# Performance work log

Hardware: AMD Instinct MI355X
Metric: run time of the kernel (lower is better)

Reference implementation:

```python
import jax, jax.numpy as jnp
import numpy as np

N_NODES = 100000
N_EDGES = 1600000
F_IN = 256
EMB = 16  # conv1 out = 2*EMB = 32, conv2 out = EMB


def setup_inputs() -> dict:
    key = jax.random.key(0)
    k1, k2, k3, k4, k5, k6, k7 = jax.random.split(key, 7)
    x = jax.random.normal(k1, (N_NODES, F_IN), dtype=jnp.float32)
    edge_index = jax.random.randint(k2, (2, N_EDGES), 0, N_NODES, dtype=jnp.int64)
    edge_weight = jax.random.uniform(k3, (N_EDGES,), dtype=jnp.float32)
    # GCNConv params: glorot-ish weights, zero bias (materialized as params)
    s1 = 1.0 / np.sqrt(F_IN)
    s2 = 1.0 / np.sqrt(2 * EMB)
    W1 = jax.random.uniform(k4, (F_IN, 2 * EMB), minval=-s1, maxval=s1, dtype=jnp.float32)
    b1 = jnp.zeros((2 * EMB,), dtype=jnp.float32)
    W2 = jax.random.uniform(k5, (2 * EMB, EMB), minval=-s2, maxval=s2, dtype=jnp.float32)
    b2 = jnp.zeros((EMB,), dtype=jnp.float32)
    return {"x": x, "edge_index": edge_index, "edge_weight": edge_weight,
            "W1": W1, "b1": b1, "W2": W2, "b2": b2}


def _gcn_norm(edge_index, edge_weight, num_nodes, dtype):
    # PyG gcn_norm with add_self_loops=True, fill_value=1.0
    row, col = edge_index[0], edge_index[1]
    loop = jnp.arange(num_nodes)
    row_a = jnp.concatenate([row, loop])
    col_a = jnp.concatenate([col, loop])
    w_a = jnp.concatenate([edge_weight, jnp.ones((num_nodes,), dtype=dtype)])
    deg = jax.ops.segment_sum(w_a, col_a, num_segments=num_nodes)
    dinv = jnp.where(deg > 0, jax.lax.rsqrt(deg), jnp.zeros_like(deg))
    norm = dinv[row_a] * w_a * dinv[col_a]
    return row_a, col_a, norm


def _gcn_conv(x, W, b, row, col, norm, num_nodes):
    h = x @ W                                  # [N, d_out] dense projection
    msg = norm[:, None] * h[row]               # gather + edge scale, [E+N, d_out]
    out = jax.ops.segment_sum(msg, col, num_segments=num_nodes)  # scatter-add
    return out + b


def reference(x, edge_index, edge_weight, W1, b1, W2, b2):
    n = x.shape[0]
    row, col, norm = _gcn_norm(edge_index, edge_weight, n, x.dtype)
    h = jax.nn.relu(_gcn_conv(x, W1, b1, row, col, norm, n))
    return _gcn_conv(h, W2, b2, row, col, norm, n)
```

## Files before the change

### kernel.cpp

```cpp
#include <hip/hip_runtime.h>
#include <hip/hip_bf16.h>

#define NN   100000
#define NE   1600000
#define FIN  256
#define HID  32
#define OUTD 16
#define NBLK ((NN + 255) / 256)

#define BM          256
#define GEMM_BLOCKS ((NN + BM - 1) / BM)
#define CNT_EDGES   2048
#define CNT_BLOCKS  ((NE + CNT_EDGES - 1) / CNT_EDGES)
#define FUSE_BLOCKS (GEMM_BLOCKS + CNT_BLOCKS)
#define FILL_BLOCKS ((NE + 1023) / 1024)

#define OFF_FLAG    0
#define OFF_DEG     64
#define OFF_DINV    (OFF_DEG + NN)
#define OFF_RANK    (OFF_DINV + NN)
#define OFF_BSUM    (OFF_RANK + NE)
#define OFF_ROWPTR  (OFF_BSUM + 1024)
#define OFF_CSR     (OFF_ROWPTR + NN + 32)
#define OFF_H1      (OFF_CSR + 2*NE)
#define OFF_P2      (OFF_H1 + NN*HID)

#define CSHIFT 26
#define CMASK  ((1u << CSHIFT) - 1u)
#define WSCALE 1048576.0f
#define WINV   (1.0f / 1048576.0f)

__device__ __forceinline__ float bf2f(unsigned short u) {
  union { unsigned int i; float f; } v; v.i = ((unsigned int)u) << 16; return v.f;
}
__device__ __forceinline__ unsigned short f2bf(float f) {
  union { float f; unsigned int i; } v; v.f = f;
  unsigned int x = v.i;
  return (unsigned short)((x + 0x7fffu + ((x >> 16) & 1u)) >> 16);
}
__device__ __forceinline__ int eidx(const int* __restrict__ ei, long long pos, int is64) {
  return is64 ? ei[2 * pos] : ei[pos];
}
__device__ __forceinline__ float ldf(const void* p, long long i, int isf32) {
  return isf32 ? ((const float*)p)[i] : bf2f(((const unsigned short*)p)[i]);
}

__global__ __launch_bounds__(256) void detect_zero_kernel(const int* __restrict__ ei,
    const unsigned short* __restrict__ xu, int* __restrict__ flags,
    unsigned int* __restrict__ zp, int zn) {
  int b = blockIdx.x;
  if (b == 0) {
    __shared__ int any, cnt;
    if (threadIdx.x == 0) { any = 0; cnt = 0; }
    __syncthreads();
    int local = 0, c = 0;
    for (int i = threadIdx.x; i < 2048; i += 256) local |= ei[2 * i + 1];
    for (int i = threadIdx.x; i < 1024; i += 256) {
      unsigned int e = (xu[2 * i] >> 7) & 0xFF;
      c += (e < 100 || e > 140) ? 1 : 0;
    }
    if (local) atomicOr(&any, 1);
    atomicAdd(&cnt, c);
    __syncthreads();
    if (threadIdx.x == 0) {
      flags[0] = (any == 0) ? 1 : 0;
      flags[1] = (cnt > 100) ? 1 : 0;
    }
  } else {
    int stride = (gridDim.x - 1) * 256;
    for (int i = (b - 1) * 256 + threadIdx.x; i < zn; i += stride) zp[i] = 0u;
  }
}

__global__ __launch_bounds__(256, 4) void count_gemm_kernel(const int* __restrict__ ei,
    const void* __restrict__ ew, unsigned int* __restrict__ deg,
    int* __restrict__ rank, const void* __restrict__ x,
    const void* __restrict__ W1, float* __restrict__ h1,
    const int* __restrict__ flags) {
  __shared__ float xs[32][BM];
  __shared__ float wl[32][36];
  int b = blockIdx.x;
  int t = threadIdx.x;

  if ((b % 3) < 2) {
    int cid = (b / 3) * 2 + (b % 3);
    int is64 = flags[0], isf32 = flags[1];
    int e0 = cid * CNT_EDGES + t;
    int c[8]; float w[8];
    #pragma unroll
    for (int q = 0; q < 8; q++) {
      int e = e0 + q * 256;
      if (e < NE) {
        c[q] = eidx(ei, (long long)NE + e, is64);
        w[q] = ldf(ew, e, isf32);
      } else c[q] = -1;
    }
    unsigned int old[8];
    #pragma unroll
    for (int q = 0; q < 8; q++) {
      if (c[q] >= 0) {
        unsigned int inc = (1u << CSHIFT) | (unsigned int)(w[q] * WSCALE + 0.5f);
        old[q] = atomicAdd(deg + c[q], inc);
      }
    }
    #pragma unroll
    for (int q = 0; q < 8; q++)
      if (c[q] >= 0) rank[e0 + q * 256] = (int)(old[q] >> CSHIFT);
    return;
  }

  int gid = b / 3;
  int rb = gid * BM;
  int isf32 = flags[1];

  int rowg = t >> 3, colg = t & 7;
  int r0 = rowg * 8, m0 = colg * 4;
  int srow = t >> 1;
  int kk0s = (t & 1) * 16;
  int kkw = t >> 3, mw = (t & 7) * 4;

  float acc[8][4];
  #pragma unroll
  for (int i = 0; i < 8; i++)
    #pragma unroll
    for (int j = 0; j < 4; j++) acc[i][j] = 0.f;

  union Pf { uint4 u[4]; float f[16]; unsigned short s[32]; };
  Pf pfx[2];
  uint4 pw;

#define LOADX(rblk, kc_) do {                                                  \
    int row_ = srow + (rblk) * 128;                                            \
    long long g_ = (long long)rb + row_;                                       \
    if (g_ < NN) {                                                             \
      if (isf32) {                                                             \
        const float* xp_ = (const float*)x + g_ * FIN + (kc_) + kk0s;          \
        pfx[rblk].u[0] = ((const uint4*)xp_)[0];                               \
        pfx[rblk].u[1] = ((const uint4*)xp_)[1];                               \
        pfx[rblk].u[2] = ((const uint4*)xp_)[2];                               \
        pfx[rblk].u[3] = ((const uint4*)xp_)[3];                               \
      } else {                                                                 \
        const unsigned short* xp_ = (const unsigned short*)x + g_ * FIN + (kc_) + kk0s; \
        pfx[rblk].u[0] = ((const uint4*)xp_)[0];                               \
        pfx[rblk].u[1] = ((const uint4*)xp_)[1];                               \
      }                                                                        \
    }                                                                          \
  } while (0)

#define STOREX(rblk) do {                                                      \
    int row_ = srow + (rblk) * 128;                                            \
    bool ok_ = ((long long)rb + row_) < NN;                                    \
    if (isf32) {                                                               \
      _Pragma("unroll")                                                        \
      for (int q = 0; q < 16; q++) xs[kk0s + q][row_] = ok_ ? pfx[rblk].f[q] : 0.f; \
    } else {                                                                   \
      _Pragma("unroll")                                                        \
      for (int q = 0; q < 16; q++) xs[kk0s + q][row_] = ok_ ? bf2f(pfx[rblk].s[q]) : 0.f; \
    }                                                                          \
  } while (0)

#define LOADW(kc_) do {                                                        \
    if (isf32) {                                                               \
      pw = *(const uint4*)((const float*)W1 + ((kc_) + kkw) * HID + mw);       \
    } else {                                                                   \
      const unsigned short* wp_ = (const unsigned short*)W1 + ((kc_) + kkw) * HID + mw; \
      pw.x = ((const unsigned int*)wp_)[0];                                    \
      pw.y = ((const unsigned int*)wp_)[1];                                    \
    }                                                                          \
  } while (0)

#define STOREW() do {                                                          \
    if (isf32) {                                                               \
      *(float4*)&wl[kkw][mw] = *(float4*)&pw;                                  \
    } else {                                                                   \
      const unsigned short* ps_ = (const unsigned short*)&pw;                  \
      wl[kkw][mw + 0] = bf2f(ps_[0]); wl[kkw][mw + 1] = bf2f(ps_[1]);          \
      wl[kkw][mw + 2] = bf2f(ps_[2]); wl[kkw][mw + 3] = bf2f(ps_[3]);          \
    }                                                                          \
  } while (0)

  LOADX(0, 0); LOADX(1, 0); LOADW(0);

  for (int kc = 0; kc < FIN; kc += 32) {
    __syncthreads();
    STOREX(0); STOREX(1); STOREW();
    __syncthreads();
    if (kc + 32 < FIN) { LOADX(0, kc + 32); LOADX(1, kc + 32); LOADW(kc + 32); }
    #pragma unroll 8
    for (int kk = 0; kk < 32; kk++) {
      float4 xa = *(const float4*)&xs[kk][r0];
      float4 xb = *(const float4*)&xs[kk][r0 + 4];
      float4 wv = *(const float4*)&wl[kk][m0];
      float xr[8] = {xa.x, xa.y, xa.z, xa.w, xb.x, xb.y, xb.z, xb.w};
      float wr[4] = {wv.x, wv.y, wv.z, wv.w};
      #pragma unroll
      for (int i = 0; i < 8; i++)
        #pragma unroll
        for (int j = 0; j < 4; j++)
          acc[i][j] = fmaf(xr[i], wr[j], acc[i][j]);
    }
  }

  #pragma unroll
  for (int i = 0; i < 8; i++) {
    int g = rb + r0 + i;
    if (g < NN) {
      float4 v; v.x = acc[i][0]; v.y = acc[i][1]; v.z = acc[i][2]; v.w = acc[i][3];
      *(float4*)(h1 + (long long)g * HID + m0) = v;
    }
  }
#undef LOADX
#undef STOREX
#undef LOADW
#undef STOREW
}

__global__ __launch_bounds__(256) void dinv_scansum_kernel(
    const unsigned int* __restrict__ deg, float* __restrict__ dinv,
    int* __restrict__ bsum) {
  int b = blockIdx.x;
  if (b < NBLK) {
    __shared__ int s[256];
    int i = b * 256 + threadIdx.x;
    s[threadIdx.x] = (i < NN) ? (int)(deg[i] >> CSHIFT) : 0;
    __syncthreads();
    for (int off = 128; off > 0; off >>= 1) {
      if (threadIdx.x < off) s[threadIdx.x] += s[threadIdx.x + off];
      __syncthreads();
    }
    if (threadIdx.x == 0) bsum[b] = s[0];
  } else {
    int i = (b - NBLK) * 256 + threadIdx.x;
    if (i >= NN) return;
    float d = (float)(deg[i] & CMASK) * WINV + 1.0f;
    dinv[i] = rsqrtf(d);
  }
}

__global__ __launch_bounds__(256) void scan_write_kernel(const unsigned int* __restrict__ deg,
    const int* __restrict__ bsum, int* __restrict__ rowptr) {
  __shared__ int a[256];
  __shared__ int base_s;
  int t = threadIdx.x;
  int b = blockIdx.x;
  int v = 0;
  for (int i = t; i < NBLK; i += 256) v += (i < b) ? bsum[i] : 0;
  a[t] = v;
  __syncthreads();
  for (int off = 128; off > 0; off >>= 1) {
    if (t < off) a[t] += a[t + off];
    __syncthreads();
  }
  if (t == 0) base_s = a[0];
  __syncthreads();
  int base = base_s;
  int i = b * 256 + t;
  int orig = (i < NN) ? (int)(deg[i] >> CSHIFT) : 0;
  a[t] = orig;
  __syncthreads();
  for (int off = 1; off < 256; off <<= 1) {
    int x2 = a[t] + ((t >= off) ? a[t - off] : 0);
    __syncthreads();
    a[t] = x2;
    __syncthreads();
  }
  if (i < NN) rowptr[i] = base + a[t] - orig;
  if (b == 0 && t == 0) rowptr[NN] = NE;
}

__global__ __launch_bounds__(256) void fill_csr_kernel(const int* __restrict__ ei,
    const void* __restrict__ ew, const float* __restrict__ dinv,
    const int* __restrict__ rowptr, const int* __restrict__ rank,
    int2* __restrict__ csr, const int* __restrict__ flags) {
  int is64 = flags[0], isf32 = flags[1];
  int e0 = blockIdx.x * 1024 + threadIdx.x;
  int r[4], c[4], rk[4]; float w[4];
  #pragma unroll
  for (int q = 0; q < 4; q++) {
    int e = e0 + q * 256;
    if (e < NE) {
      r[q]  = eidx(ei, e, is64);
      c[q]  = eidx(ei, (long long)NE + e, is64);
      w[q]  = ldf(ew, e, isf32);
      rk[q] = rank[e];
    } else c[q] = -1;
  }
  float dr[4], dc[4]; int rp[4];
  #pragma unroll
  for (int q = 0; q < 4; q++) {
    if (c[q] >= 0) {
      dr[q] = dinv[r[q]];
      dc[q] = dinv[c[q]];
      rp[q] = rowptr[c[q]];
    }
  }
  #pragma unroll
  for (int q = 0; q < 4; q++) {
    if (c[q] >= 0) {
      int2 pr; pr.x = r[q]; pr.y = __float_as_int(dr[q] * w[q] * dc[q]);
      csr[rp[q] + rk[q]] = pr;
    }
  }
}

__global__ __launch_bounds__(256) void gather1_kernel(const float* __restrict__ h1,
    const float* __restrict__ dinv, const int* __restrict__ rowptr,
    const int2* __restrict__ csr, const void* __restrict__ b1,
    const void* __restrict__ W2, float* __restrict__ p2,
    const int* __restrict__ flags) {
  __shared__ float w2lds[HID * OUTD];
  __shared__ float b1l[HID];
  __shared__ float tl[8][HID + 1];
  int t = threadIdx.x;
  int isf32 = flags[1];
  w2lds[2 * t]     = ldf(W2, 2 * t, isf32);
  w2lds[2 * t + 1] = ldf(W2, 2 * t + 1, isf32);
  if (t < HID) b1l[t] = ldf(b1, t, isf32);
  __syncthreads();

  int nl = t >> 5;
  int j  = t & 31;
  int node = blockIdx.x * 8 + nl;
  if (node < NN) {
    int k0 = rowptr[node], k1 = rowptr[node + 1];
    float acc = 0.f;
    int k = k0;
    for (; k + 8 <= k1; k += 8) {
      int2 q0 = csr[k];     int2 q1 = csr[k + 1];
      int2 q2 = csr[k + 2]; int2 q3 = csr[k + 3];
      int2 q4 = csr[k + 4]; int2 q5 = csr[k + 5];
      int2 q6 = csr[k + 6]; int2 q7 = csr[k + 7];
      float v0 = h1[q0.x * HID + j]; float v1 = h1[q1.x * HID + j];
      float v2 = h1[q2.x * HID + j]; float v3 = h1[q3.x * HID + j];
      float v4 = h1[q4.x * HID + j]; float v5 = h1[q5.x * HID + j];
      float v6 = h1[q6.x * HID + j]; float v7 = h1[q7.x * HID + j];
      acc = fmaf(__int_as_float(q0.y), v0, acc);
      acc = fmaf(__int_as_float(q1.y), v1, acc);
      acc = fmaf(__int_as_float(q2.y), v2, acc);
      acc = fmaf(__int_as_float(q3.y), v3, acc);
      acc = fmaf(__int_as_float(q4.y), v4, acc);
      acc = fmaf(__int_as_float(q5.y), v5, acc);
      acc = fmaf(__int_as_float(q6.y), v6, acc);
      acc = fmaf(__int_as_float(q7.y), v7, acc);
    }
    for (; k + 4 <= k1; k += 4) {
      int2 q0 = csr[k];     int2 q1 = csr[k + 1];
      int2 q2 = csr[k + 2]; int2 q3 = csr[k + 3];
      float v0 = h1[q0.x * HID + j]; float v1 = h1[q1.x * HID + j];
      float v2 = h1[q2.x * HID + j]; float v3 = h1[q3.x * HID + j];
      acc = fmaf(__int_as_float(q0.y), v0, acc);
      acc = fmaf(__int_as_float(q1.y), v1, acc);
      acc = fmaf(__int_as_float(q2.y), v2, acc);
      acc = fmaf(__int_as_float(q3.y), v3, acc);
    }
    for (; k < k1; k++) {
      int2 pr = csr[k];
      acc = fmaf(__int_as_float(pr.y), h1[pr.x * HID + j], acc);
    }
    float di = dinv[node];
    acc = fmaf(di * di, h1[node * HID + j], acc);
    acc += b1l[j];
    tl[nl][j] = fmaxf(acc, 0.f);
  }
  __syncthreads();
  int m = t & 31;
  if (node < NN && m < OUTD) {
    float s = 0.f;
    #pragma unroll
    for (int k = 0; k < HID; k++) s = fmaf(tl[nl][k], w2lds[k * OUTD + m], s);
    p2[node * OUTD + m] = s;
  }
}

__global__ __launch_bounds__(256) void gather2_kernel(const float* __restrict__ p2,
    const float* __restrict__ dinv, const int* __restrict__ rowptr,
    const int2* __restrict__ csr, const void* __restrict__ b2,
    void* __restrict__ out, const int* __restrict__ flags) {
  __shared__ float b2l[OUTD];
  int t = threadIdx.x;
  int isf32 = flags[1];
  if (t < OUTD) b2l[t] = ldf(b2, t, isf32);
  __syncthreads();

  int nl = t >> 4;
  int m  = t & 15;
  int node = blockIdx.x * 16 + nl;
  if (node >= NN) return;
  int k0 = rowptr[node], k1 = rowptr[node + 1];
  float acc = 0.f;
  int k = k0;
  for (; k + 8 <= k1; k += 8) {
    int2 q0 = csr[k];     int2 q1 = csr[k + 1];
    int2 q2 = csr[k + 2]; int2 q3 = csr[k + 3];
    int2 q4 = csr[k + 4]; int2 q5 = csr[k + 5];
    int2 q6 = csr[k + 6]; int2 q7 = csr[k + 7];
    float v0 = p2[q0.x * OUTD + m]; float v1 = p2[q1.x * OUTD + m];
    float v2 = p2[q2.x * OUTD + m]; float v3 = p2[q3.x * OUTD + m];
    float v4 = p2[q4.x * OUTD + m]; float v5 = p2[q5.x * OUTD + m];
    float v6 = p2[q6.x * OUTD + m]; float v7 = p2[q7.x * OUTD + m];
    acc = fmaf(__int_as_float(q0.y), v0, acc);
    acc = fmaf(__int_as_float(q1.y), v1, acc);
    acc = fmaf(__int_as_float(q2.y), v2, acc);
    acc = fmaf(__int_as_float(q3.y), v3, acc);
    acc = fmaf(__int_as_float(q4.y), v4, acc);
    acc = fmaf(__int_as_float(q5.y), v5, acc);
    acc = fmaf(__int_as_float(q6.y), v6, acc);
    acc = fmaf(__int_as_float(q7.y), v7, acc);
  }
  for (; k + 4 <= k1; k += 4) {
    int2 q0 = csr[k];     int2 q1 = csr[k + 1];
    int2 q2 = csr[k + 2]; int2 q3 = csr[k + 3];
    float v0 = p2[q0.x * OUTD + m]; float v1 = p2[q1.x * OUTD + m];
    float v2 = p2[q2.x * OUTD + m]; float v3 = p2[q3.x * OUTD + m];
    acc = fmaf(__int_as_float(q0.y), v0, acc);
    acc = fmaf(__int_as_float(q1.y), v1, acc);
    acc = fmaf(__int_as_float(q2.y), v2, acc);
    acc = fmaf(__int_as_float(q3.y), v3, acc);
  }
  for (; k < k1; k++) {
    int2 pr = csr[k];
    acc = fmaf(__int_as_float(pr.y), p2[pr.x * OUTD + m], acc);
  }
  float di = dinv[node];
  acc = fmaf(di * di, p2[node * OUTD + m], acc);
  acc += b2l[m];
  int oidx = node * OUTD + m;
  if (isf32) ((float*)out)[oidx] = acc;
  else       ((unsigned short*)out)[oidx] = f2bf(acc);
}

extern "C" void kernel_launch(void* const* d_in, const int* in_sizes, int n_in,
                              void* d_out, int out_size, void* d_ws, size_t ws_size,
                              hipStream_t stream) {
  const void* x  = d_in[0];
  const int* ei  = (const int*)d_in[1];
  const void* ew = d_in[2];
  const void* W1 = d_in[3];
  const void* b1 = d_in[4];
  const void* W2 = d_in[5];
  const void* b2 = d_in[6];
  float* ws = (float*)d_ws;
  int* wsi = (int*)d_ws;
  unsigned int* deg = (unsigned int*)(wsi + OFF_DEG);

  detect_zero_kernel<<<dim3(513), dim3(256), 0, stream>>>(ei, (const unsigned short*)x,
      wsi + OFF_FLAG, deg, NN);
  count_gemm_kernel<<<dim3(FUSE_BLOCKS), dim3(256), 0, stream>>>(ei, ew, deg,
      wsi + OFF_RANK, x, W1, ws + OFF_H1, wsi + OFF_FLAG);
  dinv_scansum_kernel<<<dim3(2 * NBLK), dim3(256), 0, stream>>>(deg, ws + OFF_DINV, wsi + OFF_BSUM);
  scan_write_kernel<<<dim3(NBLK), dim3(256), 0, stream>>>(deg, wsi + OFF_BSUM, wsi + OFF_ROWPTR);
  fill_csr_kernel<<<dim3(FILL_BLOCKS), dim3(256), 0, stream>>>(ei, ew, ws + OFF_DINV,
      wsi + OFF_ROWPTR, wsi + OFF_RANK, (int2*)(wsi + OFF_CSR), wsi + OFF_FLAG);
  gather1_kernel<<<dim3((NN + 7) / 8), dim3(256), 0, stream>>>(ws + OFF_H1, ws + OFF_DINV,
      wsi + OFF_ROWPTR, (const int2*)(wsi + OFF_CSR), b1, W2, ws + OFF_P2, wsi + OFF_FLAG);
  gather2_kernel<<<dim3((NN + 15) / 16), dim3(256), 0, stream>>>(ws + OFF_P2, ws + OFF_DINV,
      wsi + OFF_ROWPTR, (const int2*)(wsi + OFF_CSR), b2, d_out, wsi + OFF_FLAG);
}
```

Measured before the change: 381.1 us.

## Split fused count/GEMM kernel and shrink GEMM tile to 64 rows

Splits the fused degree-count and first-layer GEMM kernel into two separate kernels. The GEMM now uses 64-row tiles with a 4x2 per-thread micro-tile, padded shared memory, and launch bounds allowing 8 blocks per CU. This gives more GEMM blocks and higher occupancy in exchange for lower register reuse per thread. It also gives up the overlap of atomic counting with GEMM work and adds one kernel launch.

```diff
diff --git a/kernel.cpp b/kernel.cpp
--- a/kernel.cpp
+++ b/kernel.cpp
@@ -8,11 +8,10 @@
 #define OUTD 16
 #define NBLK ((NN + 255) / 256)
 
-#define BM          256
+#define BM          64
 #define GEMM_BLOCKS ((NN + BM - 1) / BM)
 #define CNT_EDGES   2048
 #define CNT_BLOCKS  ((NE + CNT_EDGES - 1) / CNT_EDGES)
-#define FUSE_BLOCKS (GEMM_BLOCKS + CNT_BLOCKS)
 #define FILL_BLOCKS ((NE + 1023) / 1024)
 
 #define OFF_FLAG    0
@@ -72,90 +71,80 @@
   }
 }
 
-__global__ __launch_bounds__(256, 4) void count_gemm_kernel(const int* __restrict__ ei,
+__global__ __launch_bounds__(256) void count_kernel(const int* __restrict__ ei,
     const void* __restrict__ ew, unsigned int* __restrict__ deg,
-    int* __restrict__ rank, const void* __restrict__ x,
+    int* __restrict__ rank, const int* __restrict__ flags) {
+  int t = threadIdx.x;
+  int is64 = flags[0], isf32 = flags[1];
+  int e0 = blockIdx.x * CNT_EDGES + t;
+  int c[8]; float w[8];
+  #pragma unroll
+  for (int q = 0; q < 8; q++) {
+    int e = e0 + q * 256;
+    if (e < NE) {
+      c[q] = eidx(ei, (long long)NE + e, is64);
+      w[q] = ldf(ew, e, isf32);
+    } else c[q] = -1;
+  }
+  unsigned int old[8];
+  #pragma unroll
+  for (int q = 0; q < 8; q++) {
+    if (c[q] >= 0) {
+      unsigned int inc = (1u << CSHIFT) | (unsigned int)(w[q] * WSCALE + 0.5f);
+      old[q] = atomicAdd(deg + c[q], inc);
+    }
+  }
+  #pragma unroll
+  for (int q = 0; q < 8; q++)
+    if (c[q] >= 0) rank[e0 + q * 256] = (int)(old[q] >> CSHIFT);
+}
+
+__global__ __launch_bounds__(256, 8) void gemm1_kernel(const void* __restrict__ x,
     const void* __restrict__ W1, float* __restrict__ h1,
     const int* __restrict__ flags) {
-  __shared__ float xs[32][BM];
+  __shared__ float xs[32][BM + 2];
   __shared__ float wl[32][36];
   int b = blockIdx.x;
   int t = threadIdx.x;
-
-  if ((b % 3) < 2) {
-    int cid = (b / 3) * 2 + (b % 3);
-    int is64 = flags[0], isf32 = flags[1];
-    int e0 = cid * CNT_EDGES + t;
-    int c[8]; float w[8];
-    #pragma unroll
-    for (int q = 0; q < 8; q++) {
-      int e = e0 + q * 256;
-      if (e < NE) {
-        c[q] = eidx(ei, (long long)NE + e, is64);
-        w[q] = ldf(ew, e, isf32);
-      } else c[q] = -1;
-    }
-    unsigned int old[8];
-    #pragma unroll
-    for (int q = 0; q < 8; q++) {
-      if (c[q] >= 0) {
-        unsigned int inc = (1u << CSHIFT) | (unsigned int)(w[q] * WSCALE + 0.5f);
-        old[q] = atomicAdd(deg + c[q], inc);
-      }
-    }
-    #pragma unroll
-    for (int q = 0; q < 8; q++)
-      if (c[q] >= 0) rank[e0 + q * 256] = (int)(old[q] >> CSHIFT);
-    return;
-  }
-
-  int gid = b / 3;
-  int rb = gid * BM;
+  int rb = b * BM;
   int isf32 = flags[1];
 
-  int rowg = t >> 3, colg = t & 7;
-  int r0 = rowg * 8, m0 = colg * 4;
-  int srow = t >> 1;
-  int kk0s = (t & 1) * 16;
-  int kkw = t >> 3, mw = (t & 7) * 4;
-
-  float acc[8][4];
-  #pragma unroll
-  for (int i = 0; i < 8; i++)
-    #pragma unroll
-    for (int j = 0; j < 4; j++) acc[i][j] = 0.f;
-
-  union Pf { uint4 u[4]; float f[16]; unsigned short s[32]; };
-  Pf pfx[2];
+  int j0 = (t & 15) * 2;
+  int r0 = (t >> 4) * 4;
+  int rr  = t >> 2;
+  int kk0 = (t & 3) * 8;
+  int kkw = t >> 3;
+  int mw  = (t & 7) * 4;
+  long long grow = (long long)rb + rr;
+
+  float acc[4][2];
+  #pragma unroll
+  for (int i = 0; i < 4; i++) { acc[i][0] = 0.f; acc[i][1] = 0.f; }
+
+  union Pf { uint4 u[2]; float f[8]; unsigned short s[16]; } pfx;
   uint4 pw;
 
-#define LOADX(rblk, kc_) do {                                                  \
-    int row_ = srow + (rblk) * 128;                                            \
-    long long g_ = (long long)rb + row_;                                       \
-    if (g_ < NN) {                                                             \
+#define LOADX(kc_) do {                                                        \
+    if (grow < NN) {                                                           \
       if (isf32) {                                                             \
-        const float* xp_ = (const float*)x + g_ * FIN + (kc_) + kk0s;          \
-        pfx[rblk].u[0] = ((const uint4*)xp_)[0];                               \
-        pfx[rblk].u[1] = ((const uint4*)xp_)[1];                               \
-        pfx[rblk].u[2] = ((const uint4*)xp_)[2];                               \
-        pfx[rblk].u[3] = ((const uint4*)xp_)[3];                               \
+        const float* xp_ = (const float*)x + grow * FIN + (kc_) + kk0;         \
+        pfx.u[0] = ((const uint4*)xp_)[0];                                     \
+        pfx.u[1] = ((const uint4*)xp_)[1];                                     \
       } else {                                                                 \
-        const unsigned short* xp_ = (const unsigned short*)x + g_ * FIN + (kc_) + kk0s; \
-        pfx[rblk].u[0] = ((const uint4*)xp_)[0];                               \
-        pfx[rblk].u[1] = ((const uint4*)xp_)[1];                               \
+        const unsigned short* xp_ = (const unsigned short*)x + grow * FIN + (kc_) + kk0; \
+        pfx.u[0] = *(const uint4*)xp_;                                         \
       }                                                                        \
     }                                                                          \
   } while (0)
 
-#define STOREX(rblk) do {                                                      \
-    int row_ = srow + (rblk) * 128;                                            \
-    bool ok_ = ((long long)rb + row_) < NN;                                    \
+#define STOREX() do {                                                          \
+    bool ok_ = grow < NN;                                                      \
     if (isf32) {                                                               \
       _Pragma("unroll")                                                        \
-      for (int q = 0; q < 16; q++) xs[kk0s + q][row_] = ok_ ? pfx[rblk].f[q] : 0.f; \
+      for (int q = 0; q < 8; q++) xs[kk0 + q][rr] = ok_ ? pfx.f[q] : 0.f;      \
     } else {                                                                   \
       _Pragma("unroll")                                                        \
-      for (int q = 0; q < 16; q++) xs[kk0s + q][row_] = ok_ ? bf2f(pfx[rblk].s[q]) : 0.f; \
+      for (int q = 0; q < 8; q++) xs[kk0 + q][rr] = ok_ ? bf2f(pfx.s[q]) : 0.f;\
     }                                                                          \
   } while (0)
 
@@ -179,34 +168,33 @@
     }                                                                          \
   } while (0)
 
-  LOADX(0, 0); LOADX(1, 0); LOADW(0);
+  LOADX(0); LOADW(0);
 
   for (int kc = 0; kc < FIN; kc += 32) {
     __syncthreads();
-    STOREX(0); STOREX(1); STOREW();
-    __syncthreads();
-    if (kc + 32 < FIN) { LOADX(0, kc + 32); LOADX(1, kc + 32); LOADW(kc + 32); }
+    STOREX(); STOREW();
+    __syncthreads();
+    if (kc + 32 < FIN) { LOADX(kc + 32); LOADW(kc + 32); }
     #pragma unroll 8
     for (int kk = 0; kk < 32; kk++) {
-      float4 xa = *(const float4*)&xs[kk][r0];
-      float4 xb = *(const float4*)&xs[kk][r0 + 4];
-      float4 wv = *(const float4*)&wl[kk][m0];
-      float xr[8] = {xa.x, xa.y, xa.z, xa.w, xb.x, xb.y, xb.z, xb.w};
-      float wr[4] = {wv.x, wv.y, wv.z, wv.w};
+      float2 wp2 = *(const float2*)&wl[kk][j0];
+      float2 xa = *(const float2*)&xs[kk][r0];
+      float2 xb = *(const float2*)&xs[kk][r0 + 2];
+      float xv[4] = {xa.x, xa.y, xb.x, xb.y};
       #pragma unroll
-      for (int i = 0; i < 8; i++)
-        #pragma unroll
-        for (int j = 0; j < 4; j++)
-          acc[i][j] = fmaf(xr[i], wr[j], acc[i][j]);
-    }
-  }
-
-  #pragma unroll
-  for (int i = 0; i < 8; i++) {
+      for (int i = 0; i < 4; i++) {
+        acc[i][0] = fmaf(xv[i], wp2.x, acc[i][0]);
+        acc[i][1] = fmaf(xv[i], wp2.y, acc[i][1]);
+      }
+    }
+  }
+
+  #pragma unroll
+  for (int i = 0; i < 4; i++) {
     int g = rb + r0 + i;
     if (g < NN) {
-      float4 v; v.x = acc[i][0]; v.y = acc[i][1]; v.z = acc[i][2]; v.w = acc[i][3];
-      *(float4*)(h1 + (long long)g * HID + m0) = v;
+      float2 v; v.x = acc[i][0]; v.y = acc[i][1];
+      *((float2*)(h1 + (long long)g * HID + j0)) = v;
     }
   }
 #undef LOADX
@@ -445,8 +433,10 @@
 
   detect_zero_kernel<<<dim3(513), dim3(256), 0, stream>>>(ei, (const unsigned short*)x,
       wsi + OFF_FLAG, deg, NN);
-  count_gemm_kernel<<<dim3(FUSE_BLOCKS), dim3(256), 0, stream>>>(ei, ew, deg,
-      wsi + OFF_RANK, x, W1, ws + OFF_H1, wsi + OFF_FLAG);
+  count_kernel<<<dim3(CNT_BLOCKS), dim3(256), 0, stream>>>(ei, ew, deg,
+      wsi + OFF_RANK, wsi + OFF_FLAG);
+  gemm1_kernel<<<dim3(GEMM_BLOCKS), dim3(256), 0, stream>>>(x, W1, ws + OFF_H1,
+      wsi + OFF_FLAG);
   dinv_scansum_kernel<<<dim3(2 * NBLK), dim3(256), 0, stream>>>(deg, ws + OFF_DINV, wsi + OFF_BSUM);
   scan_write_kernel<<<dim3(NBLK), dim3(256), 0, stream>>>(deg, wsi + OFF_BSUM, wsi + OFF_ROWPTR);
   fill_csr_kernel<<<dim3(FILL_BLOCKS), dim3(256), 0, stream>>>(ei, ew, ws + OFF_DINV,
```

Measured after the change: 393.0 us. +3.1%, slower.
